# Performance work log

Measured on AMD Instinct MI355X. Metric: run time of the kernel, lower is better.

Reference implementation:

```python
import jax, jax.numpy as jnp
import numpy as np

N_NODES = 100000
N_EDGES = 3200000
D_IN = 128
D_OUT = 128


def setup_inputs() -> dict:
    key = jax.random.key(0)
    k1, k2, k3, k4, k5, k6 = jax.random.split(key, 6)
    x = jax.random.normal(k1, (N_NODES, D_IN), dtype=jnp.float32)
    edge_row = jnp.sort(jax.random.randint(k2, (N_EDGES,), 0, N_NODES, dtype=jnp.int32))
    edge_col = jax.random.randint(k3, (N_EDGES,), 0, N_NODES, dtype=jnp.int32)
    edge_val = jax.random.uniform(k4, (N_EDGES,), dtype=jnp.float32)
    stdv = 1.0 / np.sqrt(D_OUT)
    weight = jax.random.uniform(k5, (D_IN, D_OUT), dtype=jnp.float32, minval=-stdv, maxval=stdv)
    bias = jax.random.uniform(k6, (D_OUT,), dtype=jnp.float32, minval=-stdv, maxval=stdv)
    return {"x": x, "edge_row": edge_row, "edge_col": edge_col,
            "edge_val": edge_val, "weight": weight, "bias": bias}


def reference(x, edge_row, edge_col, edge_val, weight, bias):
    # support = A @ x  (sparse COO SpMM via gather + segment-sum scatter)
    gathered = x[edge_col] * edge_val[:, None]          # [E, D_IN]
    support = jax.ops.segment_sum(gathered, edge_row, num_segments=N_NODES)  # [N, D_IN]
    # output = support @ W + b
    return support @ weight + bias
```

## Files before the change

kernel.cpp:

```cpp
#include <hip/hip_runtime.h>

#define NNODES 100000
#define NEDGES 3200000
#define DIM    128

typedef __bf16  bf16x8 __attribute__((ext_vector_type(8)));
typedef unsigned short u16;
typedef u16     u16x8  __attribute__((ext_vector_type(8)));
typedef float   f32x4  __attribute__((ext_vector_type(4)));
typedef unsigned int u32;
typedef u32     u32x4  __attribute__((ext_vector_type(4)));

__device__ __forceinline__ u16 f2bf(float f) {
    union { float f; unsigned int i; } c;
    c.f = f;
    unsigned int x = c.i;
    unsigned int rounding = 0x7fff + ((x >> 16) & 1);
    x += rounding;
    return (u16)(x >> 16);
}

__device__ __forceinline__ float asf(u32 u) {
    union { u32 i; float f; } c; c.i = u; return c.f;
}

__device__ __forceinline__ bf16x8 ldfrag_u16(const u16* p) {
    u16x8 u = *(const u16x8*)p;
    return __builtin_bit_cast(bf16x8, u);
}

__device__ __forceinline__ bf16x8 ldfrag_f32(const float* p) {
    f32x4 a = *(const f32x4*)p;
    f32x4 b = *(const f32x4*)(p + 4);
    u16x8 u;
#pragma unroll
    for (int i = 0; i < 4; ++i) u[i] = f2bf(a[i]);
#pragma unroll
    for (int i = 0; i < 4; ++i) u[4 + i] = f2bf(b[i]);
    return __builtin_bit_cast(bf16x8, u);
}

__global__ void build_row_ptr(const int* __restrict__ edge_row,
                              int* __restrict__ row_ptr) {
    int n = blockIdx.x * blockDim.x + threadIdx.x;
    if (n > NNODES) return;
    int lo = 0, hi = NEDGES;
    while (lo < hi) {
        int mid = (lo + hi) >> 1;
        if (edge_row[mid] < n) lo = mid + 1; else hi = mid;
    }
    row_ptr[n] = lo;
}

__global__ void prep_wt(const float* __restrict__ w, u16* __restrict__ wt) {
    int i = blockIdx.x * blockDim.x + threadIdx.x;
    if (i >= DIM * DIM) return;
    int k = i >> 7, n = i & 127;
    wt[n * DIM + k] = f2bf(w[k * DIM + n]);
}

#define WT_STRIDE 136
__global__ __launch_bounds__(256) void gemm_xw(const float* __restrict__ x,
                                               const u16* __restrict__ wt,
                                               u16* __restrict__ y) {
    __shared__ u16 wlds[DIM * WT_STRIDE];
    __shared__ u16 ybounce[4][16 * DIM];

    int tid = threadIdx.x;
    {
        const f32x4* src = (const f32x4*)wt;
#pragma unroll
        for (int i = 0; i < 8; ++i) {
            int ci  = tid + 256 * i;
            int row = ci >> 4, off = ci & 15;
            *((f32x4*)(wlds + row * WT_STRIDE) + off) = src[ci];
        }
    }
    __syncthreads();

    int wave = __builtin_amdgcn_readfirstlane(tid >> 6);
    int lane = tid & 63;
    int quad = lane >> 4, l16 = lane & 15;
    int mBase = (blockIdx.x * 4 + wave) * 16;
    if (mBase >= NNODES) return;

    const float* xrow = x + (size_t)(mBase + l16) * DIM + quad * 8;

    f32x4 acc[8];
#pragma unroll
    for (int nt = 0; nt < 8; ++nt) acc[nt] = (f32x4){0.f, 0.f, 0.f, 0.f};

#pragma unroll
    for (int kb = 0; kb < 4; ++kb) {
        bf16x8 a = ldfrag_f32(xrow + kb * 32);
#pragma unroll
        for (int nt = 0; nt < 8; ++nt) {
            bf16x8 b = ldfrag_u16(wlds + (nt * 16 + l16) * WT_STRIDE + kb * 32 + quad * 8);
            acc[nt] = __builtin_amdgcn_mfma_f32_16x16x32_bf16(a, b, acc[nt], 0, 0, 0);
        }
    }

    u16* yb = ybounce[wave];
#pragma unroll
    for (int nt = 0; nt < 8; ++nt) {
        int col = nt * 16 + l16;
#pragma unroll
        for (int r = 0; r < 4; ++r)
            yb[(quad * 4 + r) * DIM + col] = f2bf(acc[nt][r]);
    }
#pragma unroll
    for (int j = 0; j < 4; ++j) {
        int lr = j * 4 + quad;
        u16x8 t = *(const u16x8*)(yb + lr * DIM + l16 * 8);
        *(u16x8*)(y + (size_t)(mBase + lr) * DIM + l16 * 8) = t;
    }
}

__global__ __launch_bounds__(256, 8) void spmm(const int* __restrict__ row_ptr,
                                               const int* __restrict__ ecol,
                                               const float* __restrict__ eval,
                                               const u16* __restrict__ y,
                                               const float* __restrict__ bias,
                                               float* __restrict__ out) {
    int lane = threadIdx.x & 63;
    int row  = __builtin_amdgcn_readfirstlane(blockIdx.x * 4 + (threadIdx.x >> 6));
    if (row >= NNODES) return;

    int lo = row_ptr[row];
    int hi = row_ptr[row + 1];

    int grp = lane >> 4;
    int sub = lane & 15;

    float acc[8];
#pragma unroll
    for (int j = 0; j < 8; ++j) acc[j] = 0.f;

    const u16* ychunk = y + sub * 8;

    int e = lo;
    for (; e + 16 <= hi; e += 16) {
#pragma unroll
        for (int b = 0; b < 4; ++b) {
            int e0 = e + b * 4;
            int   c0 = ecol[e0], c1 = ecol[e0 + 1], c2 = ecol[e0 + 2], c3 = ecol[e0 + 3];
            float v0 = eval[e0], v1 = eval[e0 + 1], v2 = eval[e0 + 2], v3 = eval[e0 + 3];
            int   c = grp < 2 ? (grp == 0 ? c0 : c1) : (grp == 2 ? c2 : c3);
            float v = grp < 2 ? (grp == 0 ? v0 : v1) : (grp == 2 ? v2 : v3);
            u32x4 q = *(const u32x4*)(ychunk + (size_t)c * DIM);
#pragma unroll
            for (int j = 0; j < 4; ++j) {
                acc[2 * j]     += v * asf(q[j] << 16);
                acc[2 * j + 1] += v * asf(q[j] & 0xffff0000u);
            }
        }
    }
    for (; e < hi; e += 4) {
        int rem = hi - e;
        int i1 = rem > 1 ? e + 1 : e, i2 = rem > 2 ? e + 2 : e, i3 = rem > 3 ? e + 3 : e;
        int   c0 = ecol[e],  c1 = ecol[i1], c2 = ecol[i2], c3 = ecol[i3];
        float v0 = eval[e];
        float v1 = rem > 1 ? eval[i1] : 0.f;
        float v2 = rem > 2 ? eval[i2] : 0.f;
        float v3 = rem > 3 ? eval[i3] : 0.f;
        int   c = grp < 2 ? (grp == 0 ? c0 : c1) : (grp == 2 ? c2 : c3);
        float v = grp < 2 ? (grp == 0 ? v0 : v1) : (grp == 2 ? v2 : v3);
        u32x4 q = *(const u32x4*)(ychunk + (size_t)c * DIM);
#pragma unroll
        for (int j = 0; j < 4; ++j) {
            acc[2 * j]     += v * asf(q[j] << 16);
            acc[2 * j + 1] += v * asf(q[j] & 0xffff0000u);
        }
    }

#pragma unroll
    for (int j = 0; j < 8; ++j) {
        acc[j] += __shfl_xor(acc[j], 16);
        acc[j] += __shfl_xor(acc[j], 32);
    }

    if (grp == 0) {
        float* orow = out + (size_t)row * DIM + sub * 8;
        f32x4 o0, o1;
#pragma unroll
        for (int j = 0; j < 4; ++j) {
            o0[j] = acc[j]     + bias[sub * 8 + j];
            o1[j] = acc[4 + j] + bias[sub * 8 + 4 + j];
        }
        __builtin_nontemporal_store(o0, (f32x4*)orow);
        __builtin_nontemporal_store(o1, (f32x4*)(orow + 4));
    }
}

extern "C" void kernel_launch(void* const* d_in, const int* in_sizes, int n_in,
                              void* d_out, int out_size, void* d_ws, size_t ws_size,
                              hipStream_t stream) {
    const float* x        = (const float*)d_in[0];
    const int*   edge_row = (const int*)d_in[1];
    const int*   edge_col = (const int*)d_in[2];
    const float* edge_val = (const float*)d_in[3];
    const float* weight   = (const float*)d_in[4];
    const float* bias     = (const float*)d_in[5];
    float* out = (float*)d_out;

    char* ws = (char*)d_ws;
    u16* y       = (u16*)ws;
    int* row_ptr = (int*)(ws + (size_t)NNODES * DIM * 2);
    u16* wt      = (u16*)(ws + 26000128);

    prep_wt<<<(DIM * DIM + 255) / 256, 256, 0, stream>>>(weight, wt);
    build_row_ptr<<<(NNODES + 1 + 255) / 256, 256, 0, stream>>>(edge_row, row_ptr);

    gemm_xw<<<(NNODES / 16 + 3) / 4, 256, 0, stream>>>(x, wt, y);

    spmm<<<NNODES / 4, 256, 0, stream>>>(row_ptr, edge_col, edge_val, y, bias, out);
}
```

Baseline: 246.6 us.

## Split SpMM feature columns into two half-width phases with 8 edges per wave

The SpMM grid doubles and each block handles one 64-column half of the output feature dimension. Each wave now processes 8 edges at once with 8 lanes per edge instead of 4 edges with 16 lanes, which halves gather width per row and adds an extra shuffle stage. The aim is more parallelism, and possibly better cache locality when all blocks of one phase touch only half of the y table. In exchange, edge indices and values are read twice, and the per-edge gathers become 128-byte segments.

Measured after the change: 253.2 us. 2.7% more time.

```diff
diff --git a/kernel.cpp b/kernel.cpp
--- a/kernel.cpp
+++ b/kernel.cpp
@@ -122,50 +122,50 @@
                                                const u16* __restrict__ y,
                                                const float* __restrict__ bias,
                                                float* __restrict__ out) {
-    int lane = threadIdx.x & 63;
-    int row  = __builtin_amdgcn_readfirstlane(blockIdx.x * 4 + (threadIdx.x >> 6));
-    if (row >= NNODES) return;
+    int lane  = threadIdx.x & 63;
+    int wave  = threadIdx.x >> 6;
+    int bid   = blockIdx.x;
+    int phase = (bid >= (NNODES / 4)) ? 1 : 0;
+    int rb    = bid - phase * (NNODES / 4);
+    int row   = __builtin_amdgcn_readfirstlane(rb * 4 + wave);
 
     int lo = row_ptr[row];
     int hi = row_ptr[row + 1];
 
-    int grp = lane >> 4;
-    int sub = lane & 15;
+    int grp = lane >> 3;
+    int sub = lane & 7;
 
     float acc[8];
 #pragma unroll
     for (int j = 0; j < 8; ++j) acc[j] = 0.f;
 
-    const u16* ychunk = y + sub * 8;
+    const u16* ychunk = y + (size_t)phase * 64 + sub * 8;
 
     int e = lo;
     for (; e + 16 <= hi; e += 16) {
-#pragma unroll
-        for (int b = 0; b < 4; ++b) {
-            int e0 = e + b * 4;
-            int   c0 = ecol[e0], c1 = ecol[e0 + 1], c2 = ecol[e0 + 2], c3 = ecol[e0 + 3];
-            float v0 = eval[e0], v1 = eval[e0 + 1], v2 = eval[e0 + 2], v3 = eval[e0 + 3];
-            int   c = grp < 2 ? (grp == 0 ? c0 : c1) : (grp == 2 ? c2 : c3);
-            float v = grp < 2 ? (grp == 0 ? v0 : v1) : (grp == 2 ? v2 : v3);
-            u32x4 q = *(const u32x4*)(ychunk + (size_t)c * DIM);
-#pragma unroll
-            for (int j = 0; j < 4; ++j) {
-                acc[2 * j]     += v * asf(q[j] << 16);
-                acc[2 * j + 1] += v * asf(q[j] & 0xffff0000u);
-            }
-        }
-    }
-    for (; e < hi; e += 4) {
-        int rem = hi - e;
-        int i1 = rem > 1 ? e + 1 : e, i2 = rem > 2 ? e + 2 : e, i3 = rem > 3 ? e + 3 : e;
-        int   c0 = ecol[e],  c1 = ecol[i1], c2 = ecol[i2], c3 = ecol[i3];
-        float v0 = eval[e];
-        float v1 = rem > 1 ? eval[i1] : 0.f;
-        float v2 = rem > 2 ? eval[i2] : 0.f;
-        float v3 = rem > 3 ? eval[i3] : 0.f;
-        int   c = grp < 2 ? (grp == 0 ? c0 : c1) : (grp == 2 ? c2 : c3);
-        float v = grp < 2 ? (grp == 0 ? v0 : v1) : (grp == 2 ? v2 : v3);
-        u32x4 q = *(const u32x4*)(ychunk + (size_t)c * DIM);
+        int   ca = ecol[e + grp];
+        int   cb = ecol[e + 8 + grp];
+        float va = eval[e + grp];
+        float vb = eval[e + 8 + grp];
+        u32x4 qa = *(const u32x4*)(ychunk + (size_t)ca * DIM);
+        u32x4 qb = *(const u32x4*)(ychunk + (size_t)cb * DIM);
+#pragma unroll
+        for (int j = 0; j < 4; ++j) {
+            acc[2 * j]     += va * asf(qa[j] << 16);
+            acc[2 * j + 1] += va * asf(qa[j] & 0xffff0000u);
+        }
+#pragma unroll
+        for (int j = 0; j < 4; ++j) {
+            acc[2 * j]     += vb * asf(qb[j] << 16);
+            acc[2 * j + 1] += vb * asf(qb[j] & 0xffff0000u);
+        }
+    }
+    for (; e < hi; e += 8) {
+        int idx  = e + grp;
+        int live = idx < hi;
+        int   c  = ecol[live ? idx : hi - 1];
+        float v  = live ? eval[idx] : 0.f;
+        u32x4 q  = *(const u32x4*)(ychunk + (size_t)c * DIM);
 #pragma unroll
         for (int j = 0; j < 4; ++j) {
             acc[2 * j]     += v * asf(q[j] << 16);
@@ -175,17 +175,19 @@
 
 #pragma unroll
     for (int j = 0; j < 8; ++j) {
+        acc[j] += __shfl_xor(acc[j], 8);
         acc[j] += __shfl_xor(acc[j], 16);
         acc[j] += __shfl_xor(acc[j], 32);
     }
 
     if (grp == 0) {
-        float* orow = out + (size_t)row * DIM + sub * 8;
+        int   cb   = phase * 64 + sub * 8;
+        float* orow = out + (size_t)row * DIM + cb;
         f32x4 o0, o1;
 #pragma unroll
         for (int j = 0; j < 4; ++j) {
-            o0[j] = acc[j]     + bias[sub * 8 + j];
-            o1[j] = acc[4 + j] + bias[sub * 8 + 4 + j];
+            o0[j] = acc[j]     + bias[cb + j];
+            o1[j] = acc[4 + j] + bias[cb + 4 + j];
         }
         __builtin_nontemporal_store(o0, (f32x4*)orow);
         __builtin_nontemporal_store(o1, (f32x4*)(orow + 4));
@@ -213,5 +215,5 @@
 
     gemm_xw<<<(NNODES / 16 + 3) / 4, 256, 0, stream>>>(x, wt, y);
 
-    spmm<<<NNODES / 4, 256, 0, stream>>>(row_ptr, edge_col, edge_val, y, bias, out);
-}
+    spmm<<<2 * (NNODES / 4), 256, 0, stream>>>(row_ptr, edge_col, edge_val, y, bias, out);
+}
```

## Fuse weight transpose into GEMM and stage 128-row X tiles through LDS

Applied to the files above, without the earlier changes.

Removes the separate prep_wt kernel: each GEMM block now reads the fp32 weight, converts to bf16 and transposes it into LDS itself. Blocks grow to 512 threads covering 128 rows, with X loaded coalesced, converted and staged in LDS before MFMA, and the X buffer reused as the output bounce. This saves a kernel launch and improves X load coalescing, but every block redoes the weight conversion with strided LDS writes and uses more LDS per block, which may lower occupancy.

Result: slower. 260.4 us (+5.6%).

```diff
diff --git a/kernel.cpp b/kernel.cpp
--- a/kernel.cpp
+++ b/kernel.cpp
@@ -6,6 +6,7 @@
 
 typedef __bf16  bf16x8 __attribute__((ext_vector_type(8)));
 typedef unsigned short u16;
+typedef u16     u16x4  __attribute__((ext_vector_type(4)));
 typedef u16     u16x8  __attribute__((ext_vector_type(8)));
 typedef float   f32x4  __attribute__((ext_vector_type(4)));
 typedef unsigned int u32;
@@ -26,17 +27,6 @@
 
 __device__ __forceinline__ bf16x8 ldfrag_u16(const u16* p) {
     u16x8 u = *(const u16x8*)p;
-    return __builtin_bit_cast(bf16x8, u);
-}
-
-__device__ __forceinline__ bf16x8 ldfrag_f32(const float* p) {
-    f32x4 a = *(const f32x4*)p;
-    f32x4 b = *(const f32x4*)(p + 4);
-    u16x8 u;
-#pragma unroll
-    for (int i = 0; i < 4; ++i) u[i] = f2bf(a[i]);
-#pragma unroll
-    for (int i = 0; i < 4; ++i) u[4 + i] = f2bf(b[i]);
     return __builtin_bit_cast(bf16x8, u);
 }
 
@@ -52,67 +42,81 @@
     row_ptr[n] = lo;
 }
 
-__global__ void prep_wt(const float* __restrict__ w, u16* __restrict__ wt) {
-    int i = blockIdx.x * blockDim.x + threadIdx.x;
-    if (i >= DIM * DIM) return;
-    int k = i >> 7, n = i & 127;
-    wt[n * DIM + k] = f2bf(w[k * DIM + n]);
-}
-
 #define WT_STRIDE 136
-__global__ __launch_bounds__(256) void gemm_xw(const float* __restrict__ x,
-                                               const u16* __restrict__ wt,
-                                               u16* __restrict__ y) {
+__global__ __launch_bounds__(512, 4) void gemm_xw(const float* __restrict__ x,
+                                                  const float* __restrict__ w,
+                                                  u16* __restrict__ y) {
     __shared__ u16 wlds[DIM * WT_STRIDE];
-    __shared__ u16 ybounce[4][16 * DIM];
+    __shared__ u16 xlds[128 * WT_STRIDE];
 
     int tid = threadIdx.x;
-    {
-        const f32x4* src = (const f32x4*)wt;
-#pragma unroll
-        for (int i = 0; i < 8; ++i) {
-            int ci  = tid + 256 * i;
-            int row = ci >> 4, off = ci & 15;
-            *((f32x4*)(wlds + row * WT_STRIDE) + off) = src[ci];
-        }
+    int rowBase = blockIdx.x * 128;
+
+#pragma unroll
+    for (int i = 0; i < 8; ++i) {
+        int ci  = tid + 512 * i;
+        int r   = ci >> 5;
+        int off = ci & 31;
+        if (rowBase + r < NNODES) {
+            f32x4 v = *(const f32x4*)(x + (size_t)(rowBase + r) * DIM + off * 4);
+            u16x4 b;
+#pragma unroll
+            for (int j = 0; j < 4; ++j) b[j] = f2bf(v[j]);
+            *(u16x4*)(xlds + r * WT_STRIDE + off * 4) = b;
+        }
+    }
+
+#pragma unroll
+    for (int i = 0; i < 8; ++i) {
+        int ci = tid + 512 * i;
+        int k  = ci >> 5;
+        int n0 = (ci & 31) * 4;
+        f32x4 v = *(const f32x4*)(w + (size_t)k * DIM + n0);
+#pragma unroll
+        for (int j = 0; j < 4; ++j)
+            wlds[(n0 + j) * WT_STRIDE + k] = f2bf(v[j]);
     }
     __syncthreads();
 
     int wave = __builtin_amdgcn_readfirstlane(tid >> 6);
     int lane = tid & 63;
     int quad = lane >> 4, l16 = lane & 15;
-    int mBase = (blockIdx.x * 4 + wave) * 16;
-    if (mBase >= NNODES) return;
-
-    const float* xrow = x + (size_t)(mBase + l16) * DIM + quad * 8;
+    int mBase = rowBase + wave * 16;
+    int active = (mBase < NNODES);
 
     f32x4 acc[8];
 #pragma unroll
     for (int nt = 0; nt < 8; ++nt) acc[nt] = (f32x4){0.f, 0.f, 0.f, 0.f};
 
-#pragma unroll
-    for (int kb = 0; kb < 4; ++kb) {
-        bf16x8 a = ldfrag_f32(xrow + kb * 32);
+    if (active) {
+#pragma unroll
+        for (int kb = 0; kb < 4; ++kb) {
+            bf16x8 a = ldfrag_u16(xlds + (wave * 16 + l16) * WT_STRIDE + kb * 32 + quad * 8);
+#pragma unroll
+            for (int nt = 0; nt < 8; ++nt) {
+                bf16x8 b = ldfrag_u16(wlds + (nt * 16 + l16) * WT_STRIDE + kb * 32 + quad * 8);
+                acc[nt] = __builtin_amdgcn_mfma_f32_16x16x32_bf16(a, b, acc[nt], 0, 0, 0);
+            }
+        }
+    }
+
+    __syncthreads();
+
+    if (active) {
+        u16* yb = xlds + wave * (16 * DIM);
 #pragma unroll
         for (int nt = 0; nt < 8; ++nt) {
-            bf16x8 b = ldfrag_u16(wlds + (nt * 16 + l16) * WT_STRIDE + kb * 32 + quad * 8);
-            acc[nt] = __builtin_amdgcn_mfma_f32_16x16x32_bf16(a, b, acc[nt], 0, 0, 0);
-        }
-    }
-
-    u16* yb = ybounce[wave];
-#pragma unroll
-    for (int nt = 0; nt < 8; ++nt) {
-        int col = nt * 16 + l16;
-#pragma unroll
-        for (int r = 0; r < 4; ++r)
-            yb[(quad * 4 + r) * DIM + col] = f2bf(acc[nt][r]);
-    }
-#pragma unroll
-    for (int j = 0; j < 4; ++j) {
-        int lr = j * 4 + quad;
-        u16x8 t = *(const u16x8*)(yb + lr * DIM + l16 * 8);
-        *(u16x8*)(y + (size_t)(mBase + lr) * DIM + l16 * 8) = t;
+            int col = nt * 16 + l16;
+#pragma unroll
+            for (int r = 0; r < 4; ++r)
+                yb[(quad * 4 + r) * DIM + col] = f2bf(acc[nt][r]);
+        }
+#pragma unroll
+        for (int j = 0; j < 4; ++j) {
+            int lr = j * 4 + quad;
+            u16x8 t = *(const u16x8*)(yb + lr * DIM + l16 * 8);
+            *(u16x8*)(y + (size_t)(mBase + lr) * DIM + l16 * 8) = t;
+        }
     }
 }
 
@@ -206,12 +210,10 @@
     char* ws = (char*)d_ws;
     u16* y       = (u16*)ws;
     int* row_ptr = (int*)(ws + (size_t)NNODES * DIM * 2);
-    u16* wt      = (u16*)(ws + 26000128);
-
-    prep_wt<<<(DIM * DIM + 255) / 256, 256, 0, stream>>>(weight, wt);
+
     build_row_ptr<<<(NNODES + 1 + 255) / 256, 256, 0, stream>>>(edge_row, row_ptr);
 
-    gemm_xw<<<(NNODES / 16 + 3) / 4, 256, 0, stream>>>(x, wt, y);
+    gemm_xw<<<(NNODES + 127) / 128, 512, 0, stream>>>(x, weight, y);
 
     spmm<<<NNODES / 4, 256, 0, stream>>>(row_ptr, edge_col, edge_val, y, bias, out);
 }
```
